# Kernel optimization log

Measured on AMD Instinct MI355X. Metric: run time of the kernel, lower is better.

The kernel has to match this reference:

```python
import jax, jax.numpy as jnp
import numpy as np

H = 8      # heads
DK = 64    # k_size
DV = 128   # output_size // heads
DIN = 1024 # input_size


def setup_inputs() -> dict:
    key = jax.random.key(0)
    ks = jax.random.split(key, 10)
    B, C = 4, 2048
    p = lambda k, sh: jax.random.normal(k, sh, jnp.float32) * 0.02
    return {
        "x": jax.random.normal(ks[0], (B, C, DIN), jnp.float32),
        "mask": jax.random.normal(ks[1], (B, C), jnp.float32),
        "Mq_w": p(ks[2], (H * DK, DIN)), "Mq_b": p(ks[3], (H * DK,)),
        "Mk_w": p(ks[4], (H * DK, DIN)), "Mk_b": p(ks[5], (H * DK,)),
        "Mv_w": p(ks[6], (H * DV, DIN)), "Mv_b": p(ks[7], (H * DV,)),
        "Wo_w": p(ks[8], (H * DV, H * DV)), "Wo_b": p(ks[9], (H * DV,)),
    }


def reference(x, mask, Mq_w, Mq_b, Mk_w, Mk_b, Mv_w, Mv_b, Wo_w, Wo_b):
    B, C, _ = x.shape
    # torch .view(B, heads, C, -1) on a [B, C, H*D] tensor is a FLAT reshape
    # (not a transpose) -- replicated here verbatim.
    q = (x @ Mq_w.T + Mq_b).reshape(B, H, C, DK)
    k = (x @ Mk_w.T + Mk_b).reshape(B, H, C, DK)
    v = (x @ Mv_w.T + Mv_b).reshape(B, H, C, DV)
    scores = jnp.einsum('bhqd,bhkd->bhqk', q, k)            # [B,H,C,C]
    # mask is added per-QUERY position (unsqueeze(-1)), before the 1/sqrt(dk) scale
    scores = scores + mask[:, None, :, None]
    # original softmaxes over dim=1 of [B*H, C, C] == the query axis (axis=2 here)
    att = jax.nn.softmax(scores / jnp.sqrt(jnp.float32(DK)), axis=2)
    out = jnp.einsum('bhqk,bhkd->bhqd', att, v)              # [B,H,C,DV]
    out = out.reshape(B, C, H * DV)                          # flat reshape, as in .view(B, C, -1)
    return out @ Wo_w.T + Wo_b
```

## Files before the change

kernel.cpp:

```cpp
#include <hip/hip_runtime.h>
#include <hip/hip_bf16.h>
#include <cstdint>
#include <cstddef>

constexpr int Cc = 2048;
constexpr int Mrows = 8192;
constexpr float SC2 = 0.18033688011112042f;

typedef __attribute__((ext_vector_type(8))) short short8;
typedef __attribute__((ext_vector_type(4))) float floatx4;
typedef unsigned short us;

#define MFMA_BF16(a, b, c) __builtin_amdgcn_mfma_f32_16x16x32_bf16((a), (b), (c), 0, 0, 0)
#define EXP2F(x) __builtin_amdgcn_exp2f(x)

__device__ __forceinline__ us f2bf(float f) {
  union { float f; unsigned u; } v; v.f = f;
  unsigned r = v.u + 0x7fffu + ((v.u >> 16) & 1u);
  return (us)(r >> 16);
}
__device__ __forceinline__ float bf2f(us u) {
  union { unsigned u; float f; } v; v.u = ((unsigned)u) << 16;
  return v.f;
}
__device__ __forceinline__ uint2 pack4bf(float e0, float e1, float e2, float e3) {
  union { __hip_bfloat162 h; unsigned u; } a, b;
  a.h = __float22bfloat162_rn(float2{e0, e1});
  b.h = __float22bfloat162_rn(float2{e2, e3});
  return uint2{a.u, b.u};
}
__device__ __forceinline__ void async16(const us* g, us* l) {
  __builtin_amdgcn_global_load_lds(
      (const __attribute__((address_space(1))) unsigned int*)(g),
      (__attribute__((address_space(3))) unsigned int*)(l), 16, 0, 0);
}

__global__ __launch_bounds__(256) void cast_all(
    const float* __restrict__ x,  const float* __restrict__ mq,
    const float* __restrict__ mk, const float* __restrict__ mv,
    const float* __restrict__ wo,
    us* __restrict__ xb, us* __restrict__ wqb, us* __restrict__ wkb,
    us* __restrict__ wvb, us* __restrict__ wob)
{
  size_t i = ((size_t)blockIdx.x * 256 + threadIdx.x) * 8;
  const float* src; us* dst; size_t j;
  if      (i <  8388608) { src = x;  dst = xb;  j = i; }
  else if (i <  8912896) { src = mq; dst = wqb; j = i -  8388608; }
  else if (i <  9437184) { src = mk; dst = wkb; j = i -  8912896; }
  else if (i < 10485760) { src = mv; dst = wvb; j = i -  9437184; }
  else if (i < 11534336) { src = wo; dst = wob; j = i - 10485760; }
  else return;
  float4 a = *(const float4*)(src + j);
  float4 b = *(const float4*)(src + j + 4);
  short8 o;
  o[0] = (short)f2bf(a.x); o[1] = (short)f2bf(a.y);
  o[2] = (short)f2bf(a.z); o[3] = (short)f2bf(a.w);
  o[4] = (short)f2bf(b.x); o[5] = (short)f2bf(b.y);
  o[6] = (short)f2bf(b.z); o[7] = (short)f2bf(b.w);
  *(short8*)(dst + j) = o;
}

__global__ __launch_bounds__(256, 3) void gemm_qkv(
    const us* __restrict__ A, const us* __restrict__ Wall,
    const float* __restrict__ bq, const float* __restrict__ bk,
    const float* __restrict__ bv,
    us* __restrict__ Qo, us* __restrict__ Ko, us* __restrict__ Vo)
{
  __shared__ __align__(16) us As[128 * 64];
  __shared__ __align__(16) us Ws[128 * 64];
  const int t = threadIdx.x, lane = t & 63, wid = t >> 6;
  const int wr = wid >> 1, wc = wid & 1;
  const int quad = lane >> 4, l15 = lane & 15, l7 = l15 & 7;
  const int id = blockIdx.x;
  const int nt = (id & 7) * 2 + ((id >> 3) & 1);
  const int mt = id >> 4;
  const int m0 = mt * 128, n0 = nt * 128;
  const int K = 1024;

  floatx4 acc[4][4];
#pragma unroll
  for (int i = 0; i < 4; i++)
#pragma unroll
    for (int j = 0; j < 4; j++) acc[i][j] = (floatx4){0.f, 0.f, 0.f, 0.f};

  for (int k0 = 0; k0 < K; k0 += 64) {
    __syncthreads();
#pragma unroll
    for (int j = 0; j < 4; j++) {
      int f = (wid * 4 + j) * 64 + lane;
      int row = f >> 3, sc = (f & 7) ^ (row & 7);
      async16(A    + (size_t)(m0 + row) * K + k0 + sc * 8, &As[f * 8]);
      async16(Wall + (size_t)(n0 + row) * K + k0 + sc * 8, &Ws[f * 8]);
    }
    __syncthreads();
    short8 aF[4][2], bF[4][2];
#pragma unroll
    for (int fm = 0; fm < 4; fm++) {
      int ra = wr * 64 + fm * 16 + l15;
      int rb = wc * 64 + fm * 16 + l15;
#pragma unroll
      for (int c = 0; c < 2; c++) {
        aF[fm][c] = *(const short8*)&As[ra * 64 + (((c << 2) + quad) ^ l7) * 8];
        bF[fm][c] = *(const short8*)&Ws[rb * 64 + (((c << 2) + quad) ^ l7) * 8];
      }
    }
#pragma unroll
    for (int i = 0; i < 4; i++)
#pragma unroll
      for (int j = 0; j < 4; j++) {
        floatx4 d = MFMA_BF16(aF[i][0], bF[j][0], acc[i][j]);
        acc[i][j] = MFMA_BF16(aF[i][1], bF[j][1], d);
      }
  }

  us* dst; const float* bias; int Nout, c0;
  if (nt < 4)      { dst = Qo; bias = bq; Nout = 512;  c0 = n0; }
  else if (nt < 8) { dst = Ko; bias = bk; Nout = 512;  c0 = n0 - 512; }
  else             { dst = Vo; bias = bv; Nout = 1024; c0 = n0 - 1024; }

#pragma unroll
  for (int fn = 0; fn < 4; fn++) {
    int col = c0 + wc * 64 + fn * 16 + l15;
    float bvv = bias[col];
#pragma unroll
    for (int fm = 0; fm < 4; fm++)
#pragma unroll
      for (int r = 0; r < 4; r++) {
        int m = m0 + wr * 64 + fm * 16 + quad * 4 + r;
        dst[(size_t)m * Nout + col] = f2bf(acc[fm][fn][r] + bvv);
      }
  }
}

__global__ __launch_bounds__(256, 3) void gemm_out(
    const us* __restrict__ A, const us* __restrict__ W,
    const float* __restrict__ bias, float* __restrict__ outp)
{
  __shared__ __align__(16) us As[128 * 64];
  __shared__ __align__(16) us Ws[128 * 64];
  const int t = threadIdx.x, lane = t & 63, wid = t >> 6;
  const int wr = wid >> 1, wc = wid & 1;
  const int quad = lane >> 4, l15 = lane & 15, l7 = l15 & 7;
  const int id = blockIdx.x;
  const int m0 = (id >> 3) * 128, n0 = (id & 7) * 128;
  const int K = 1024, N = 1024;

  floatx4 acc[4][4];
#pragma unroll
  for (int i = 0; i < 4; i++)
#pragma unroll
    for (int j = 0; j < 4; j++) acc[i][j] = (floatx4){0.f, 0.f, 0.f, 0.f};

  for (int k0 = 0; k0 < K; k0 += 64) {
    __syncthreads();
#pragma unroll
    for (int j = 0; j < 4; j++) {
      int f = (wid * 4 + j) * 64 + lane;
      int row = f >> 3, sc = (f & 7) ^ (row & 7);
      async16(A + (size_t)(m0 + row) * K + k0 + sc * 8, &As[f * 8]);
      async16(W + (size_t)(n0 + row) * K + k0 + sc * 8, &Ws[f * 8]);
    }
    __syncthreads();
    short8 aF[4][2], bF[4][2];
#pragma unroll
    for (int fm = 0; fm < 4; fm++) {
      int ra = wr * 64 + fm * 16 + l15;
      int rb = wc * 64 + fm * 16 + l15;
#pragma unroll
      for (int c = 0; c < 2; c++) {
        aF[fm][c] = *(const short8*)&As[ra * 64 + (((c << 2) + quad) ^ l7) * 8];
        bF[fm][c] = *(const short8*)&Ws[rb * 64 + (((c << 2) + quad) ^ l7) * 8];
      }
    }
#pragma unroll
    for (int i = 0; i < 4; i++)
#pragma unroll
      for (int j = 0; j < 4; j++) {
        floatx4 d = MFMA_BF16(aF[i][0], bF[j][0], acc[i][j]);
        acc[i][j] = MFMA_BF16(aF[i][1], bF[j][1], d);
      }
  }

#pragma unroll
  for (int fn = 0; fn < 4; fn++) {
    int col = n0 + wc * 64 + fn * 16 + l15;
    float bvv = bias[col];
#pragma unroll
    for (int fm = 0; fm < 4; fm++)
#pragma unroll
      for (int r = 0; r < 4; r++) {
        int m = m0 + wr * 64 + fm * 16 + quad * 4 + r;
        outp[(size_t)m * N + col] = acc[fm][fn][r] + bvv;
      }
  }
}

__global__ __launch_bounds__(256, 2) void attn_pass1(
    const us* __restrict__ Q_, const us* __restrict__ K_,
    const float* __restrict__ mask, float* __restrict__ invZ)
{
  __shared__ __align__(16) us Qs[2][128 * 64];
  const int t = threadIdx.x, lane = t & 63, wid = t >> 6;
  const int quad = lane >> 4, l15 = lane & 15, l7 = l15 & 7;
  const int id = blockIdx.x;
  const int bh = (id & 7) * 4 + ((id >> 3) & 3);
  const int kt = (id >> 5) * 128;
  const int b = bh >> 3;
  const us* Kb = K_ + (size_t)bh * Cc * 64;
  const us* Qb = Q_ + (size_t)bh * Cc * 64;
  const float* mrow = mask + (size_t)b * Cc;

  short8 kA[2][2];
#pragma unroll
  for (int kf = 0; kf < 2; kf++)
#pragma unroll
    for (int c = 0; c < 2; c++)
      kA[kf][c] = *(const short8*)(Kb + (size_t)(kt + wid * 32 + kf * 16 + l15) * 64 + c * 32 + quad * 8);

  float zacc[2][4] = {};

#pragma unroll
  for (int j = 0; j < 4; j++) {
    int f = (wid * 4 + j) * 64 + lane;
    int row = f >> 3, sc = (f & 7) ^ (row & 7);
    async16(Qb + (size_t)row * 64 + sc * 8, &Qs[0][f * 8]);
  }
  __syncthreads();

  int p = 0;
  for (int it = 0; it < 16; it++) {
    if (it + 1 < 16) {
#pragma unroll
      for (int j = 0; j < 4; j++) {
        int f = (wid * 4 + j) * 64 + lane;
        int row = f >> 3, sc = (f & 7) ^ (row & 7);
        async16(Qb + (size_t)((it + 1) * 128 + row) * 64 + sc * 8, &Qs[1 - p][f * 8]);
      }
    }
    const us* Qsp = Qs[p];
#pragma unroll
    for (int qf = 0; qf < 8; qf++) {
      int row = qf * 16 + l15;
      short8 q0 = *(const short8*)&Qsp[row * 64 + ((quad) ^ l7) * 8];
      short8 q1 = *(const short8*)&Qsp[row * 64 + ((4 + quad) ^ l7) * 8];
      float mv = mrow[it * 128 + qf * 16 + l15] * SC2;
#pragma unroll
      for (int kf = 0; kf < 2; kf++) {
        floatx4 d = (floatx4){0.f, 0.f, 0.f, 0.f};
        d = MFMA_BF16(kA[kf][0], q0, d);
        d = MFMA_BF16(kA[kf][1], q1, d);
#pragma unroll
        for (int r = 0; r < 4; r++)
          zacc[kf][r] += EXP2F(fmaf(d[r], SC2, mv));
      }
    }
    __syncthreads();
    p ^= 1;
  }

#pragma unroll
  for (int kf = 0; kf < 2; kf++)
#pragma unroll
    for (int r = 0; r < 4; r++) {
      float v = zacc[kf][r];
      v += __shfl_xor(v, 1); v += __shfl_xor(v, 2);
      v += __shfl_xor(v, 4); v += __shfl_xor(v, 8);
      if (l15 == 0)
        invZ[(size_t)bh * Cc + kt + wid * 32 + kf * 16 + quad * 4 + r] = 1.0f / v;
    }
}

__global__ __launch_bounds__(256) void transpose_v(
    const us* __restrict__ V, const float* __restrict__ invZ,
    us* __restrict__ VT)
{
  __shared__ __align__(16) us Vs[32][136];
  __shared__ float izs[32];
  const int bh = blockIdx.y, ct = blockIdx.x * 32;
  const int t = threadIdx.x;
  const us* Vb  = V  + (size_t)bh * Cc * 128;
  us*       VTb = VT + (size_t)bh * 128 * Cc;
#pragma unroll
  for (int i = 0; i < 2; i++) {
    int idx = t + i * 256, c = idx >> 4, d0 = (idx & 15) * 8;
    *(short8*)&Vs[c][d0] = *(const short8*)(Vb + (size_t)(ct + c) * 128 + d0);
  }
  if (t < 32) izs[t] = invZ[(size_t)bh * Cc + ct + t];
  __syncthreads();
#pragma unroll
  for (int i = 0; i < 2; i++) {
    int idx = t + i * 256, dv = idx >> 2, cb = (idx & 3) * 8;
    short8 o;
#pragma unroll
    for (int j = 0; j < 8; j++)
      o[j] = (short)f2bf(bf2f(Vs[cb + j][dv]) * izs[cb + j]);
    *(short8*)(VTb + (size_t)dv * Cc + ct + cb) = o;
  }
}

__global__ __launch_bounds__(256, 2) void attn_pass2(
    const us* __restrict__ Q_, const us* __restrict__ K_,
    const us* __restrict__ VT_, const float* __restrict__ mask,
    us* __restrict__ Ab)
{
  __shared__ __align__(16) us VTs[2][128 * 64];
  __shared__ __align__(16) us Ps[2][128 * 64];
  const int t = threadIdx.x, lane = t & 63, wid = t >> 6;
  const int quad = lane >> 4, l15 = lane & 15, l7 = l15 & 7;
  const int id = blockIdx.x;
  const int bh = (id & 7) * 4 + ((id >> 3) & 3);
  const int qt = (id >> 5) * 128;
  const int b = bh >> 3;
  const us* Qb  = Q_  + (size_t)bh * Cc * 64;
  const us* Kb  = K_  + (size_t)bh * Cc * 64;
  const us* VTb = VT_ + (size_t)bh * 128 * Cc;

  const int kHalf = wid & 1, qHalfS = wid >> 1;
  const int qPV = wid & 1, dvPV = wid >> 1;

  short8 qB[4][2];
  float mv2[4];
#pragma unroll
  for (int qq = 0; qq < 4; qq++) {
    int q = qt + qHalfS * 64 + qq * 16 + l15;
#pragma unroll
    for (int c = 0; c < 2; c++)
      qB[qq][c] = *(const short8*)(Qb + (size_t)q * 64 + c * 32 + quad * 8);
    mv2[qq] = mask[(size_t)b * Cc + q] * SC2;
  }

  floatx4 acc[4][4];
#pragma unroll
  for (int i = 0; i < 4; i++)
#pragma unroll
    for (int j = 0; j < 4; j++) acc[i][j] = (floatx4){0.f, 0.f, 0.f, 0.f};

  short8 kA[2][2];
#pragma unroll
  for (int kk = 0; kk < 2; kk++)
#pragma unroll
    for (int c = 0; c < 2; c++)
      kA[kk][c] = *(const short8*)(Kb + (size_t)((kHalf * 2 + kk) * 16 + l15) * 64 + c * 32 + quad * 8);

#pragma unroll
  for (int j = 0; j < 4; j++) {
    int f = (wid * 4 + j) * 64 + lane;
    int row = f >> 3, sc = (f & 7) ^ (row & 7);
    async16(VTb + (size_t)row * Cc + sc * 8, &VTs[0][f * 8]);
  }

#pragma unroll
  for (int kk = 0; kk < 2; kk++) {
    int kf = kHalf * 2 + kk;
#pragma unroll
    for (int qq = 0; qq < 4; qq++) {
      floatx4 d = (floatx4){0.f, 0.f, 0.f, 0.f};
      d = MFMA_BF16(kA[kk][0], qB[qq][0], d);
      d = MFMA_BF16(kA[kk][1], qB[qq][1], d);
      uint2 pk = pack4bf(EXP2F(fmaf(d[0], SC2, mv2[qq])),
                         EXP2F(fmaf(d[1], SC2, mv2[qq])),
                         EXP2F(fmaf(d[2], SC2, mv2[qq])),
                         EXP2F(fmaf(d[3], SC2, mv2[qq])));
      int prow = qHalfS * 64 + qq * 16 + l15;
      *(uint2*)&Ps[0][prow * 64 + (((kf << 1) + (quad >> 1)) ^ l7) * 8 + (quad & 1) * 4] = pk;
    }
  }
#pragma unroll
  for (int kk = 0; kk < 2; kk++)
#pragma unroll
    for (int c = 0; c < 2; c++)
      kA[kk][c] = *(const short8*)(Kb + (size_t)(64 + (kHalf * 2 + kk) * 16 + l15) * 64 + c * 32 + quad * 8);
  __syncthreads();

  int p = 0, s = 0;
  for (int kb = 0; kb < Cc; kb += 64) {
    if (kb + 64 < Cc) {
#pragma unroll
      for (int j = 0; j < 4; j++) {
        int f = (wid * 4 + j) * 64 + lane;
        int row = f >> 3, sc = (f & 7) ^ (row & 7);
        async16(VTb + (size_t)row * Cc + kb + 64 + sc * 8, &VTs[1 - p][f * 8]);
      }
#pragma unroll
      for (int kk = 0; kk < 2; kk++) {
        int kf = kHalf * 2 + kk;
#pragma unroll
        for (int qq = 0; qq < 4; qq++) {
          floatx4 d = (floatx4){0.f, 0.f, 0.f, 0.f};
          d = MFMA_BF16(kA[kk][0], qB[qq][0], d);
          d = MFMA_BF16(kA[kk][1], qB[qq][1], d);
          uint2 pk = pack4bf(EXP2F(fmaf(d[0], SC2, mv2[qq])),
                             EXP2F(fmaf(d[1], SC2, mv2[qq])),
                             EXP2F(fmaf(d[2], SC2, mv2[qq])),
                             EXP2F(fmaf(d[3], SC2, mv2[qq])));
          int prow = qHalfS * 64 + qq * 16 + l15;
          *(uint2*)&Ps[1 - s][prow * 64 + (((kf << 1) + (quad >> 1)) ^ l7) * 8 + (quad & 1) * 4] = pk;
        }
      }
      if (kb + 128 < Cc) {
#pragma unroll
        for (int kk = 0; kk < 2; kk++)
#pragma unroll
          for (int c = 0; c < 2; c++)
            kA[kk][c] = *(const short8*)(Kb + (size_t)(kb + 128 + (kHalf * 2 + kk) * 16 + l15) * 64 + c * 32 + quad * 8);
      }
    }

    short8 pA[4][2];
#pragma unroll
    for (int qq = 0; qq < 4; qq++) {
      int prow = qPV * 64 + qq * 16 + l15;
#pragma unroll
      for (int kc = 0; kc < 2; kc++)
        pA[qq][kc] = *(const short8*)&Ps[s][prow * 64 + (((kc << 2) + quad) ^ l7) * 8];
    }
#pragma unroll
    for (int fn = 0; fn < 4; fn++) {
      int vrow = dvPV * 64 + fn * 16 + l15;
#pragma unroll
      for (int kc = 0; kc < 2; kc++) {
        short8 vB = *(const short8*)&VTs[p][vrow * 64 + (((kc << 2) + quad) ^ l7) * 8];
#pragma unroll
        for (int qq = 0; qq < 4; qq++)
          acc[qq][fn] = MFMA_BF16(pA[qq][kc], vB, acc[qq][fn]);
      }
    }
    __syncthreads();
    p ^= 1; s ^= 1;
  }

#pragma unroll
  for (int qq = 0; qq < 4; qq++)
#pragma unroll
    for (int fn = 0; fn < 4; fn++)
#pragma unroll
      for (int r = 0; r < 4; r++) {
        int q = qt + qPV * 64 + qq * 16 + quad * 4 + r;
        int dv = dvPV * 64 + fn * 16 + l15;
        Ab[((size_t)bh * Cc + q) * 128 + dv] = f2bf(acc[qq][fn][r]);
      }
}

extern "C" void kernel_launch(void* const* d_in, const int* in_sizes, int n_in,
                              void* d_out, int out_size, void* d_ws, size_t ws_size,
                              hipStream_t stream)
{
  const float* x    = (const float*)d_in[0];
  const float* mask = (const float*)d_in[1];
  const float* Mq_w = (const float*)d_in[2];
  const float* Mq_b = (const float*)d_in[3];
  const float* Mk_w = (const float*)d_in[4];
  const float* Mk_b = (const float*)d_in[5];
  const float* Mv_w = (const float*)d_in[6];
  const float* Mv_b = (const float*)d_in[7];
  const float* Wo_w = (const float*)d_in[8];
  const float* Wo_b = (const float*)d_in[9];
  float* outp = (float*)d_out;

  us* xb  = (us*)d_ws;
  us* wq  = xb  + 8388608;
  us* wk  = wq  + 524288;
  us* wv  = wk  + 524288;
  us* wo  = wv  + 1048576;
  us* Qb  = wo  + 1048576;
  us* Kb  = Qb  + 4194304;
  us* Vb  = Kb  + 4194304;
  us* VTb = Vb  + 8388608;
  us* Ab  = VTb + 8388608;
  float* invZ = (float*)(Ab + 8388608);

  cast_all<<<5632, 256, 0, stream>>>(x, Mq_w, Mk_w, Mv_w, Wo_w, xb, wq, wk, wv, wo);

  gemm_qkv<<<1024, 256, 0, stream>>>(xb, wq, Mq_b, Mk_b, Mv_b, Qb, Kb, Vb);

  attn_pass1<<<512, 256, 0, stream>>>(Qb, Kb, mask, invZ);
  transpose_v<<<dim3(64, 32), 256, 0, stream>>>(Vb, invZ, VTb);
  attn_pass2<<<512, 256, 0, stream>>>(Qb, Kb, VTb, mask, Ab);

  gemm_out<<<512, 256, 0, stream>>>(Ab, wo, Wo_b, outp);
}
```

Before: 289.7 us.

## Halve pass1 key tile and read V directly from global in pass2

New measurement: 337.7 us. 16.6% more time.

```diff
diff --git a/kernel.cpp b/kernel.cpp
--- a/kernel.cpp
+++ b/kernel.cpp
@@ -195,7 +195,7 @@
   }
 }
 
-__global__ __launch_bounds__(256, 2) void attn_pass1(
+__global__ __launch_bounds__(256, 4) void attn_pass1(
     const us* __restrict__ Q_, const us* __restrict__ K_,
     const float* __restrict__ mask, float* __restrict__ invZ)
 {
@@ -204,20 +204,18 @@
   const int quad = lane >> 4, l15 = lane & 15, l7 = l15 & 7;
   const int id = blockIdx.x;
   const int bh = (id & 7) * 4 + ((id >> 3) & 3);
-  const int kt = (id >> 5) * 128;
+  const int kt = (id >> 5) * 64;
   const int b = bh >> 3;
   const us* Kb = K_ + (size_t)bh * Cc * 64;
   const us* Qb = Q_ + (size_t)bh * Cc * 64;
   const float* mrow = mask + (size_t)b * Cc;
 
-  short8 kA[2][2];
-#pragma unroll
-  for (int kf = 0; kf < 2; kf++)
-#pragma unroll
-    for (int c = 0; c < 2; c++)
-      kA[kf][c] = *(const short8*)(Kb + (size_t)(kt + wid * 32 + kf * 16 + l15) * 64 + c * 32 + quad * 8);
-
-  float zacc[2][4] = {};
+  short8 kA[2];
+#pragma unroll
+  for (int c = 0; c < 2; c++)
+    kA[c] = *(const short8*)(Kb + (size_t)(kt + wid * 16 + l15) * 64 + c * 32 + quad * 8);
+
+  float zacc[4] = {};
 
 #pragma unroll
   for (int j = 0; j < 4; j++) {
@@ -244,30 +242,25 @@
       short8 q0 = *(const short8*)&Qsp[row * 64 + ((quad) ^ l7) * 8];
       short8 q1 = *(const short8*)&Qsp[row * 64 + ((4 + quad) ^ l7) * 8];
       float mv = mrow[it * 128 + qf * 16 + l15] * SC2;
-#pragma unroll
-      for (int kf = 0; kf < 2; kf++) {
-        floatx4 d = (floatx4){0.f, 0.f, 0.f, 0.f};
-        d = MFMA_BF16(kA[kf][0], q0, d);
-        d = MFMA_BF16(kA[kf][1], q1, d);
-#pragma unroll
-        for (int r = 0; r < 4; r++)
-          zacc[kf][r] += EXP2F(fmaf(d[r], SC2, mv));
-      }
+      floatx4 d = (floatx4){0.f, 0.f, 0.f, 0.f};
+      d = MFMA_BF16(kA[0], q0, d);
+      d = MFMA_BF16(kA[1], q1, d);
+#pragma unroll
+      for (int r = 0; r < 4; r++)
+        zacc[r] += EXP2F(fmaf(d[r], SC2, mv));
     }
     __syncthreads();
     p ^= 1;
   }
 
 #pragma unroll
-  for (int kf = 0; kf < 2; kf++)
-#pragma unroll
-    for (int r = 0; r < 4; r++) {
-      float v = zacc[kf][r];
-      v += __shfl_xor(v, 1); v += __shfl_xor(v, 2);
-      v += __shfl_xor(v, 4); v += __shfl_xor(v, 8);
-      if (l15 == 0)
-        invZ[(size_t)bh * Cc + kt + wid * 32 + kf * 16 + quad * 4 + r] = 1.0f / v;
-    }
+  for (int r = 0; r < 4; r++) {
+    float v = zacc[r];
+    v += __shfl_xor(v, 1); v += __shfl_xor(v, 2);
+    v += __shfl_xor(v, 4); v += __shfl_xor(v, 8);
+    if (l15 == 0)
+      invZ[(size_t)bh * Cc + kt + wid * 16 + quad * 4 + r] = 1.0f / v;
+  }
 }
 
 __global__ __launch_bounds__(256) void transpose_v(
@@ -298,12 +291,11 @@
   }
 }
 
-__global__ __launch_bounds__(256, 2) void attn_pass2(
+__global__ __launch_bounds__(256, 3) void attn_pass2(
     const us* __restrict__ Q_, const us* __restrict__ K_,
     const us* __restrict__ VT_, const float* __restrict__ mask,
     us* __restrict__ Ab)
 {
-  __shared__ __align__(16) us VTs[2][128 * 64];
   __shared__ __align__(16) us Ps[2][128 * 64];
   const int t = threadIdx.x, lane = t & 63, wid = t >> 6;
   const int quad = lane >> 4, l15 = lane & 15, l7 = l15 & 7;
@@ -343,13 +335,6 @@
       kA[kk][c] = *(const short8*)(Kb + (size_t)((kHalf * 2 + kk) * 16 + l15) * 64 + c * 32 + quad * 8);
 
 #pragma unroll
-  for (int j = 0; j < 4; j++) {
-    int f = (wid * 4 + j) * 64 + lane;
-    int row = f >> 3, sc = (f & 7) ^ (row & 7);
-    async16(VTb + (size_t)row * Cc + sc * 8, &VTs[0][f * 8]);
-  }
-
-#pragma unroll
   for (int kk = 0; kk < 2; kk++) {
     int kf = kHalf * 2 + kk;
 #pragma unroll
@@ -372,15 +357,9 @@
       kA[kk][c] = *(const short8*)(Kb + (size_t)(64 + (kHalf * 2 + kk) * 16 + l15) * 64 + c * 32 + quad * 8);
   __syncthreads();
 
-  int p = 0, s = 0;
+  int s = 0;
   for (int kb = 0; kb < Cc; kb += 64) {
     if (kb + 64 < Cc) {
-#pragma unroll
-      for (int j = 0; j < 4; j++) {
-        int f = (wid * 4 + j) * 64 + lane;
-        int row = f >> 3, sc = (f & 7) ^ (row & 7);
-        async16(VTb + (size_t)row * Cc + kb + 64 + sc * 8, &VTs[1 - p][f * 8]);
-      }
 #pragma unroll
       for (int kk = 0; kk < 2; kk++) {
         int kf = kHalf * 2 + kk;
@@ -416,17 +395,17 @@
     }
 #pragma unroll
     for (int fn = 0; fn < 4; fn++) {
-      int vrow = dvPV * 64 + fn * 16 + l15;
+      const us* vrow = VTb + (size_t)(dvPV * 64 + fn * 16 + l15) * Cc + kb;
 #pragma unroll
       for (int kc = 0; kc < 2; kc++) {
-        short8 vB = *(const short8*)&VTs[p][vrow * 64 + (((kc << 2) + quad) ^ l7) * 8];
+        short8 vB = *(const short8*)(vrow + kc * 32 + quad * 8);
 #pragma unroll
         for (int qq = 0; qq < 4; qq++)
           acc[qq][fn] = MFMA_BF16(pA[qq][kc], vB, acc[qq][fn]);
       }
     }
     __syncthreads();
-    p ^= 1; s ^= 1;
+    s ^= 1;
   }
 
 #pragma unroll
@@ -473,7 +452,7 @@
 
   gemm_qkv<<<1024, 256, 0, stream>>>(xb, wq, Mq_b, Mk_b, Mv_b, Qb, Kb, Vb);
 
-  attn_pass1<<<512, 256, 0, stream>>>(Qb, Kb, mask, invZ);
+  attn_pass1<<<1024, 256, 0, stream>>>(Qb, Kb, mask, invZ);
   transpose_v<<<dim3(64, 32), 256, 0, stream>>>(Vb, invZ, VTb);
   attn_pass2<<<512, 256, 0, stream>>>(Qb, Kb, VTb, mask, Ab);
 
```
